# Kernel optimization log

Measured on AMD Instinct MI355X. Metric: run time of the kernel, lower is better.

The kernel has to match this reference:

```python
import jax, jax.numpy as jnp
import numpy as np

# ---- static config (seq_lens / is_prefill are Python lists in the original) ----
HIDDEN, H, D = 4096, 32, 128
SEQ = 1024            # prefill length / decode history length
N_PRE, N_DEC = 4, 4
T = N_PRE * SEQ + N_DEC            # 4100 total tokens
SEQ_LENS = [SEQ] * N_PRE + [SEQ] * N_DEC
IS_PREFILL = [True] * N_PRE + [False] * N_DEC
NUM_SLOTS = 8192
MAX_LEN, ROPE_BASE = 8192, 10000.0
SCALE = D ** -0.5


def _rope_tables():
    inv_freq = 1.0 / (ROPE_BASE ** (np.arange(0, D, 2, dtype=np.float32) / D))
    t = np.arange(MAX_LEN, dtype=np.float32)
    freqs = np.outer(t, inv_freq)
    emb = np.concatenate([freqs, freqs], axis=-1)  # [MAX_LEN, D]
    return jnp.asarray(np.cos(emb), jnp.float32), jnp.asarray(np.sin(emb), jnp.float32)

COS_T, SIN_T = _rope_tables()


def rotate_half(x):
    x1, x2 = jnp.split(x, 2, axis=-1)
    return jnp.concatenate([-x2, x1], axis=-1)


def setup_inputs() -> dict:
    key = jax.random.key(0)
    k1, k2, k3 = jax.random.split(key, 3)
    x = jax.random.normal(k1, (T, HIDDEN), jnp.float32)
    # positions: prefill seqs get 0..SEQ-1, decode seqs are at position SEQ
    pos = np.concatenate([np.tile(np.arange(SEQ), N_PRE), np.full(N_DEC, SEQ)]).astype(np.int64)
    positions = jnp.asarray(pos)
    slot_mapping = jnp.arange(T, dtype=jnp.int64)
    k_cache = jnp.zeros((NUM_SLOTS, H, D), jnp.float32)
    v_cache = jnp.zeros((NUM_SLOTS, H, D), jnp.float32)
    w_qkv = jax.random.normal(k2, (HIDDEN, 3 * H * D), jnp.float32) * 0.02
    w_out = jax.random.normal(k3, (H * D, HIDDEN), jnp.float32) * 0.02
    return {"x": x, "k_cache": k_cache, "v_cache": v_cache, "w_qkv": w_qkv,
            "w_out": w_out, "positions": positions, "slot_mapping": slot_mapping}


def reference(x, k_cache, v_cache, w_qkv, w_out, positions, slot_mapping):
    qkv = x @ w_qkv                                   # [T, 3*H*D]
    q, k, v = jnp.split(qkv, 3, axis=-1)
    q = q.reshape(T, H, D)
    k = k.reshape(T, H, D)
    v = v.reshape(T, H, D)
    cos = COS_T[positions][:, None, :]                # [T, 1, D]
    sin = SIN_T[positions][:, None, :]
    q = q * cos + rotate_half(q) * sin
    k = k * cos + rotate_half(k) * sin
    # scatter new k/v into flat paged cache
    kc = k_cache.at[slot_mapping].set(k)
    vc = v_cache.at[slot_mapping].set(v)

    outs = []
    off = 0
    for seq_len, prefill in zip(SEQ_LENS, IS_PREFILL):
        nq = seq_len if prefill else 1
        q_i = q[off:off + nq]                         # [nq, H, D]
        if prefill:
            k_i, v_i = k[off:off + nq], v[off:off + nq]
            attn = jnp.einsum('qhd,khd->hqk', q_i, k_i) * SCALE
            mask = jnp.triu(jnp.full((nq, nq), -jnp.inf, jnp.float32), 1)
            attn = jax.nn.softmax(attn + mask, axis=-1)
            out = jnp.einsum('hqk,khd->qhd', attn, v_i).reshape(nq, H * D)
        else:
            k_h, v_h = kc[:seq_len], vc[:seq_len]     # history from cache
            attn = jnp.einsum('qhd,khd->hqk', q_i, k_h) * SCALE
            attn = jax.nn.softmax(attn, axis=-1)
            out = jnp.einsum('hqk,khd->qhd', attn, v_h).reshape(1, H * D)
        outs.append(out)
        off += nq
    return jnp.concatenate(outs, axis=0) @ w_out      # [T, HIDDEN]
```

## Files before the change

### kernel.cpp

```cpp
#include <hip/hip_runtime.h>

#define T_TOK 4100
#define MMAIN 4096
#define HID   4096
#define NH    32
#define DH    128
#define NQKV  12288
#define ATT_SCALE 0.08838834764831845f
#define NEG_BIG  (-3.0e38f)

typedef unsigned short ushort_t;
typedef __attribute__((ext_vector_type(8))) short bf16x8;
typedef __attribute__((ext_vector_type(4))) float f32x4;

typedef const void __attribute__((address_space(1)))* gas_ptr;
typedef void __attribute__((address_space(3)))* las_ptr;

__device__ __forceinline__ ushort_t f2bf(float f){
  unsigned int u = __builtin_bit_cast(unsigned int, f);
  u = u + 0x7FFFu + ((u >> 16) & 1u);
  return (ushort_t)(u >> 16);
}
__device__ __forceinline__ float bf2f(ushort_t h){
  unsigned int u = ((unsigned int)h) << 16;
  return __builtin_bit_cast(float, u);
}
__device__ __forceinline__ f32x4 mfma16(bf16x8 a, bf16x8 b, f32x4 c){
  return __builtin_amdgcn_mfma_f32_16x16x32_bf16(a, b, c, 0, 0, 0);
}
__device__ __forceinline__ void gload_lds16(const void* g, void* l){
  __builtin_amdgcn_global_load_lds((gas_ptr)g, (las_ptr)l, 16, 0, 0);
}


__global__ void convert_x(const float* __restrict__ x, ushort_t* __restrict__ xb){
  const long nvec = (long)T_TOK * HID / 4;
  for (long i4 = (long)blockIdx.x * 256 + threadIdx.x; i4 < nvec; i4 += 2048L * 256){
    const long i = i4 * 4;
    const float4 v = *(const float4*)(x + i);
    union { ushort_t u[4]; uint2 w; } o;
    o.u[0] = f2bf(v.x); o.u[1] = f2bf(v.y); o.u[2] = f2bf(v.z); o.u[3] = f2bf(v.w);
    *(uint2*)(xb + i) = o.w;
  }
}

__global__ void tconv(const float* __restrict__ W, ushort_t* __restrict__ WT, int R, int C){
  __shared__ float tile[64][65];
  const int bc = blockIdx.x, br = blockIdx.y;
  const int tid = threadIdx.x;
  const int c4 = tid & 15, r0 = tid >> 4;
  const long cbase = (long)bc * 64 + c4 * 4;
#pragma unroll
  for (int j = 0; j < 4; ++j){
    const int r = r0 + j*16;
    const float4 v = *(const float4*)(W + ((long)br*64 + r) * C + cbase);
    tile[r][c4*4+0] = v.x; tile[r][c4*4+1] = v.y;
    tile[r][c4*4+2] = v.z; tile[r][c4*4+3] = v.w;
  }
  __syncthreads();
  const int c = tid >> 2, rseg = (tid & 3) * 16;
  union { ushort_t u[16]; uint4 w[2]; } o;
#pragma unroll
  for (int e = 0; e < 16; ++e) o.u[e] = f2bf(tile[rseg + e][c]);
  ushort_t* dst = WT + ((long)bc*64 + c) * R + (long)br*64 + rseg;
  *(uint4*)(dst)     = o.w[0];
  *(uint4*)(dst + 8) = o.w[1];
}


#define MFMAQ(QM,QN,BARR)                                                         \
  _Pragma("unroll")                                                               \
  for (int mi = 0; mi < 4; ++mi) {                                                \
    _Pragma("unroll")                                                             \
    for (int ni = 0; ni < 2; ++ni) {                                              \
      acc[QM][QN][mi][ni] = mfma16(af[mi][0], BARR[ni][0], acc[QM][QN][mi][ni]);  \
      acc[QM][QN][mi][ni] = mfma16(af[mi][1], BARR[ni][1], acc[QM][QN][mi][ni]);  \
    } }

template<bool OUT_BF16>
__global__ void __launch_bounds__(512, 2)
gemm256(const ushort_t* __restrict__ A, const ushort_t* __restrict__ B,
        ushort_t* __restrict__ Cb, float* __restrict__ Cf,
        int N, int K, int GM, int Mvalid)
{
  extern __shared__ char smem[];
  char* smA = smem;
  char* smB = smem + 65536;

  const int nwg = gridDim.x;
  int bid = blockIdx.x;
  bid = (bid & 7) * (nwg >> 3) + (bid >> 3);
  const int bm = bid % GM, bn = bid / GM;

  const int tid = threadIdx.x;
  const int wid = tid >> 6, lane = tid & 63;
  const int wm = wid >> 2, wn = wid & 3;
  const int l16 = lane & 15, g = lane >> 4;
  const int lr = lane >> 3, lu = lane & 7;

  const long arow0 = (long)bm * 256;
  const long brow0 = (long)bn * 256;

  const ushort_t* aS[4]; const ushort_t* bS[4];
#pragma unroll
  for (int cc = 0; cc < 4; ++cc){
    aS[cc] = A + (arow0 + cc*64 + wid*8 + lr) * (long)K + (lu ^ lr) * 8;
    bS[cc] = B + (brow0 + cc*64 + wid*8 + lr) * (long)K + (lu ^ lr) * 8;
  }

  auto stageA = [&](int buf, int cc, long kt){
    gload_lds16(aS[cc] + kt, smA + buf*32768 + (cc*64 + wid*8)*128);
  };
  auto stageB = [&](int buf, int cc, long kt){
    gload_lds16(bS[cc] + kt, smB + buf*32768 + (cc*64 + wid*8)*128);
  };
  auto ldA = [&](int buf, int qm, int mi, int ks) -> bf16x8 {
    const int row = qm*128 + wm*64 + mi*16 + l16;
    return *(const bf16x8*)(smA + buf*32768 + row*128 + (((ks*4+g) ^ (l16&7))*16));
  };
  auto ldB = [&](int buf, int qn, int ni, int ks) -> bf16x8 {
    const int row = qn*128 + wn*32 + ni*16 + l16;
    return *(const bf16x8*)(smB + buf*32768 + row*128 + (((ks*4+g) ^ (l16&7))*16));
  };

  f32x4 acc[2][2][4][2];
#pragma unroll
  for (int a_ = 0; a_ < 2; ++a_)
#pragma unroll
  for (int b_ = 0; b_ < 2; ++b_)
#pragma unroll
  for (int c_ = 0; c_ < 4; ++c_)
#pragma unroll
  for (int d_ = 0; d_ < 2; ++d_) acc[a_][b_][c_][d_] = (f32x4){0.f,0.f,0.f,0.f};

  bf16x8 af[4][2], bf0[2][2], bf1[2][2];
  const int NT = K >> 6;

  stageA(0,0,0); stageA(0,1,0);
  stageB(0,0,0); stageB(0,1,0);
  stageB(0,2,0); stageB(0,3,0);
  stageA(0,2,0); stageA(0,3,0);
  asm volatile("s_waitcnt vmcnt(4)" ::: "memory");
  __builtin_amdgcn_s_barrier();

  auto tile = [&](int buf, long ktn){
    asm volatile("s_waitcnt vmcnt(2)" ::: "memory");
#pragma unroll
    for (int mi = 0; mi < 4; ++mi){ af[mi][0] = ldA(buf,0,mi,0); af[mi][1] = ldA(buf,0,mi,1); }
#pragma unroll
    for (int ni = 0; ni < 2; ++ni){ bf0[ni][0] = ldB(buf,0,ni,0); bf0[ni][1] = ldB(buf,0,ni,1); }
    stageA(buf^1, 0, ktn); stageA(buf^1, 1, ktn);
    __builtin_amdgcn_s_barrier();
    asm volatile("s_waitcnt lgkmcnt(0)" ::: "memory");
    __builtin_amdgcn_sched_barrier(0);
    __builtin_amdgcn_s_setprio(1);
    MFMAQ(0,0,bf0);
    __builtin_amdgcn_s_setprio(0);
    asm volatile("s_waitcnt vmcnt(2)" ::: "memory");
#pragma unroll
    for (int ni = 0; ni < 2; ++ni){ bf1[ni][0] = ldB(buf,1,ni,0); bf1[ni][1] = ldB(buf,1,ni,1); }
    stageB(buf^1, 0, ktn); stageB(buf^1, 1, ktn);
    __builtin_amdgcn_s_barrier();
    asm volatile("s_waitcnt lgkmcnt(0)" ::: "memory");
    __builtin_amdgcn_sched_barrier(0);
    __builtin_amdgcn_s_setprio(1);
    MFMAQ(0,1,bf1);
    __builtin_amdgcn_s_setprio(0);
#pragma unroll
    for (int mi = 0; mi < 4; ++mi){ af[mi][0] = ldA(buf,1,mi,0); af[mi][1] = ldA(buf,1,mi,1); }
    stageB(buf^1, 2, ktn); stageB(buf^1, 3, ktn);
    __builtin_amdgcn_s_barrier();
    asm volatile("s_waitcnt lgkmcnt(0)" ::: "memory");
    __builtin_amdgcn_sched_barrier(0);
    __builtin_amdgcn_s_setprio(1);
    MFMAQ(1,1,bf1);
    __builtin_amdgcn_s_setprio(0);
    asm volatile("s_waitcnt vmcnt(2)" ::: "memory");
    stageA(buf^1, 2, ktn); stageA(buf^1, 3, ktn);
    __builtin_amdgcn_s_barrier();
    __builtin_amdgcn_sched_barrier(0);
    __builtin_amdgcn_s_setprio(1);
    MFMAQ(1,0,bf0);
    __builtin_amdgcn_s_setprio(0);
  };

  for (int t = 0; t < NT; t += 2){
    const long k1 = (long)(t+1) * 64;
    const long k2 = (long)((t+2 < NT) ? (t+2) : (NT-1)) * 64;
    tile(0, k1);
    tile(1, k2);
  }
  asm volatile("s_waitcnt vmcnt(0)" ::: "memory");

#pragma unroll
  for (int qm = 0; qm < 2; ++qm)
#pragma unroll
  for (int qn = 0; qn < 2; ++qn)
#pragma unroll
  for (int mi = 0; mi < 4; ++mi)
#pragma unroll
  for (int ni = 0; ni < 2; ++ni)
#pragma unroll
  for (int r = 0; r < 4; ++r){
    const long row = arow0 + qm*128 + wm*64 + mi*16 + g*4 + r;
    const long col = brow0 + qn*128 + wn*32 + ni*16 + l16;
    if (OUT_BF16){
      Cb[row * N + col] = f2bf(acc[qm][qn][mi][ni][r]);
    } else {
      if (row < Mvalid) Cf[row * N + col] = acc[qm][qn][mi][ni][r];
    }
  }
}


__global__ void __launch_bounds__(256, 8)
gemv_tail(const ushort_t* __restrict__ A, const ushort_t* __restrict__ B,
          ushort_t* __restrict__ Cb, float* __restrict__ Cf, int ldc)
{
  const int col  = blockIdx.x * 4 + (threadIdx.x >> 6);
  const int lane = threadIdx.x & 63;
  const ushort_t* brow  = B + (long)col * HID + lane * 64;
  const ushort_t* abase = A + 4096L * HID + lane * 64;
  float acc0 = 0.f, acc1 = 0.f, acc2 = 0.f, acc3 = 0.f;
#pragma unroll
  for (int i = 0; i < 8; ++i){
    union { bf16x8 v; short s[8]; } bv, a0, a1, a2, a3;
    bv.v = *(const bf16x8*)(brow + i*8);
    a0.v = *(const bf16x8*)(abase + 0L*HID + i*8);
    a1.v = *(const bf16x8*)(abase + 1L*HID + i*8);
    a2.v = *(const bf16x8*)(abase + 2L*HID + i*8);
    a3.v = *(const bf16x8*)(abase + 3L*HID + i*8);
#pragma unroll
    for (int e = 0; e < 8; ++e){
      const float bf_ = bf2f((ushort_t)bv.s[e]);
      acc0 += bf2f((ushort_t)a0.s[e]) * bf_;
      acc1 += bf2f((ushort_t)a1.s[e]) * bf_;
      acc2 += bf2f((ushort_t)a2.s[e]) * bf_;
      acc3 += bf2f((ushort_t)a3.s[e]) * bf_;
    }
  }
#pragma unroll
  for (int off = 32; off; off >>= 1){
    acc0 += __shfl_xor(acc0, off);
    acc1 += __shfl_xor(acc1, off);
    acc2 += __shfl_xor(acc2, off);
    acc3 += __shfl_xor(acc3, off);
  }
  if (lane == 0){
    if (Cb){
      Cb[4096L*ldc + col] = f2bf(acc0);
      Cb[4097L*ldc + col] = f2bf(acc1);
      Cb[4098L*ldc + col] = f2bf(acc2);
      Cb[4099L*ldc + col] = f2bf(acc3);
    } else {
      Cf[4096L*ldc + col] = acc0;
      Cf[4097L*ldc + col] = acc1;
      Cf[4098L*ldc + col] = acc2;
      Cf[4099L*ldc + col] = acc3;
    }
  }
}


__global__ void rope_scatter(ushort_t* __restrict__ qkv,
                             const int* __restrict__ pos32,
                             const int* __restrict__ slot32,
                             ushort_t* __restrict__ kcw, ushort_t* __restrict__ vcw)
{
  const long gi = (long)blockIdx.x * 256 + threadIdx.x;
  if (gi >= (long)T_TOK * NH * 8) return;
  const int  i8 = gi & 7;
  const int  h  = (gi >> 3) & 31;
  const long t  = gi >> 8;

  const bool p64 = (pos32[1] == 0);
  const bool s64 = (slot32[1] == 0);
  const long pv   = p64 ? ((const long long*)pos32)[t]  : (long)pos32[t];
  const long slot = s64 ? ((const long long*)slot32)[t] : (long)slot32[t];

  float cs[8], sn[8];
#pragma unroll
  for (int e = 0; e < 8; ++e){
    const int i = i8*8 + e;
    const float inv = exp2f(-(float)i * 0.2076187116f);
    __sincosf((float)pv * inv, &sn[e], &cs[e]);
  }

  ushort_t* base = qkv + t * (long)NQKV + h * DH + i8*8;
  {
    union { bf16x8 v; short s[8]; } lo, hi;
    lo.v = *(const bf16x8*)(base);
    hi.v = *(const bf16x8*)(base + 64);
#pragma unroll
    for (int e = 0; e < 8; ++e){
      const float a = bf2f((ushort_t)lo.s[e]), b = bf2f((ushort_t)hi.s[e]);
      lo.s[e] = (short)f2bf(a * cs[e] - b * sn[e]);
      hi.s[e] = (short)f2bf(b * cs[e] + a * sn[e]);
    }
    *(bf16x8*)(base)      = lo.v;
    *(bf16x8*)(base + 64) = hi.v;
  }

  if (t < 4096){
    ushort_t* kb = base + HID;
    union { bf16x8 v; short s[8]; } lo, hi;
    lo.v = *(const bf16x8*)(kb);
    hi.v = *(const bf16x8*)(kb + 64);
#pragma unroll
    for (int e = 0; e < 8; ++e){
      const float a = bf2f((ushort_t)lo.s[e]), b = bf2f((ushort_t)hi.s[e]);
      lo.s[e] = (short)f2bf(a * cs[e] - b * sn[e]);
      hi.s[e] = (short)f2bf(b * cs[e] + a * sn[e]);
    }
    *(bf16x8*)(kb)      = lo.v;
    *(bf16x8*)(kb + 64) = hi.v;

    if (slot >= 0 && slot < 1024){
      ushort_t* kd = kcw + (slot * NH + h) * DH + i8*8;
      *(bf16x8*)(kd)      = lo.v;
      *(bf16x8*)(kd + 64) = hi.v;
      const ushort_t* vsrc = base + 2 * HID;
      ushort_t* vd = vcw + (slot * NH + h) * DH + i8*8;
      *(bf16x8*)(vd)      = *(const bf16x8*)(vsrc);
      *(bf16x8*)(vd + 64) = *(const bf16x8*)(vsrc + 64);
    }
  }
}


__global__ void __launch_bounds__(256, 3)
attn_fused(const ushort_t* __restrict__ qkv, const ushort_t* __restrict__ kcw,
           const ushort_t* __restrict__ vcw, ushort_t* __restrict__ attn)
{
  __shared__ char sm[44032];
  const int qb = blockIdx.x, h = blockIdx.y, sq = blockIdx.z;
  const int tid = threadIdx.x, wid = tid >> 6, lane = tid & 63;

  if (qb == 16){
    float* qs  = (float*)sm;
    float* ps  = qs + 128;
    float* red = ps + 1024;
    float* oh  = red + 8;
    const long t = 4096 + sq;
    if (tid < 128) qs[tid] = bf2f(qkv[t * (long)NQKV + h*DH + tid]);
    __syncthreads();
    float sv[4];
#pragma unroll
    for (int j = 0; j < 4; j++){
      const int key = tid + j*256;
      const ushort_t* kr = kcw + ((long)key * NH + h) * DH;
      float acc = 0.f;
      for (int d = 0; d < 128; d += 8){
        union { bf16x8 v; short s8[8]; } uu;
        uu.v = *(const bf16x8*)(kr + d);
#pragma unroll
        for (int e = 0; e < 8; e++) acc += qs[d+e] * bf2f((ushort_t)uu.s8[e]);
      }
      sv[j] = acc * ATT_SCALE;
    }
    float mx = fmaxf(fmaxf(sv[0], sv[1]), fmaxf(sv[2], sv[3]));
#pragma unroll
    for (int off = 1; off < 64; off <<= 1) mx = fmaxf(mx, __shfl_xor(mx, off));
    if (lane == 0) red[wid] = mx;
    __syncthreads();
    const float gmax = fmaxf(fmaxf(red[0], red[1]), fmaxf(red[2], red[3]));
    float psum = 0.f;
#pragma unroll
    for (int j = 0; j < 4; j++){
      const float p = __expf(sv[j] - gmax);
      ps[tid + j*256] = p;
      psum += p;
    }
#pragma unroll
    for (int off = 1; off < 64; off <<= 1) psum += __shfl_xor(psum, off);
    if (lane == 0) red[4 + wid] = psum;
    __syncthreads();
    const float gsum = red[4] + red[5] + red[6] + red[7];
    const int d = tid & 127, half = tid >> 7;
    float acc = 0.f;
    for (int key = half*512; key < half*512 + 512; ++key)
      acc += ps[key] * bf2f(vcw[((long)key * NH + h) * DH + d]);
    if (half) oh[d] = acc;
    __syncthreads();
    if (!half) attn[t * HID + h*DH + d] = f2bf((acc + oh[d]) / gsum);
    return;
  }

  ushort_t (*Ks)[128]    = (ushort_t(*)[128])sm;
  ushort_t (*Vt)[72]     = (ushort_t(*)[72])(sm + 16384);
  ushort_t (*Ps)[16][72] = (ushort_t(*)[16][72])(sm + 34816);
  const long tok0 = (long)sq * 1024;
  const int l16 = lane & 15, g = lane >> 4;
  const int q0 = qb * 64;

  bf16x8 qf[4];
  {
    const ushort_t* qrow = qkv + (tok0 + q0 + wid*16 + l16) * (long)NQKV + h * DH;
#pragma unroll
    for (int dc = 0; dc < 4; ++dc) qf[dc] = *(const bf16x8*)(qrow + dc*32 + g*8);
  }

  bf16x8 vones;
  {
    union { ushort_t u[8]; bf16x8 v; } one_;
#pragma unroll
    for (int e = 0; e < 8; ++e) one_.u[e] = 0x3F80;
    vones = one_.v;
  }

  f32x4 oacc[8];
#pragma unroll
  for (int i = 0; i < 8; i++) oacc[i] = (f32x4){0.f, 0.f, 0.f, 0.f};
  f32x4 lacc = (f32x4){0.f, 0.f, 0.f, 0.f};

  const int nkb = qb + 1;
  for (int kb = 0; kb < nkb; ++kb){
    __syncthreads();
    {
      const ushort_t* kbase = qkv + (tok0 + kb*64) * (long)NQKV + HID + h * DH;
#pragma unroll
      for (int c = 0; c < 4; ++c){
        const int row = c*16 + wid*4 + g;
        const int pu = (l16 & 8) | ((l16 ^ (row & 7)) & 7);
        gload_lds16(kbase + (long)row * NQKV + pu*8, &Ks[c*16 + wid*4][0]);
      }
    }
    {
      const int key4 = (tid & 15) * 4;
      const int dg8  = tid >> 4;
      const ushort_t* vbase = qkv + (tok0 + kb*64) * (long)NQKV + 2*HID + h*DH + dg8*8;
      union { bf16x8 v; short s8[8]; } vr[4];
#pragma unroll
      for (int j = 0; j < 4; ++j)
        vr[j].v = *(const bf16x8*)(vbase + (long)(key4 + j) * NQKV);
#pragma unroll
      for (int e = 0; e < 8; ++e){
        union { ushort_t u[4]; uint2 w; } o;
        o.u[0] = (ushort_t)vr[0].s8[e]; o.u[1] = (ushort_t)vr[1].s8[e];
        o.u[2] = (ushort_t)vr[2].s8[e]; o.u[3] = (ushort_t)vr[3].s8[e];
        *(uint2*)&Vt[dg8*8 + e][key4] = o.w;
      }
    }
    __syncthreads();

    {
      f32x4 sfr[4];
#pragma unroll
      for (int nf = 0; nf < 4; ++nf) sfr[nf] = (f32x4){0.f,0.f,0.f,0.f};
      __builtin_amdgcn_s_setprio(1);
#pragma unroll
      for (int nf = 0; nf < 4; ++nf){
#pragma unroll
        for (int dc = 0; dc < 4; ++dc){
          const int uu = dc*4 + g;
          const int pu = (uu & 8) | ((uu ^ (l16 & 7)) & 7);
          bf16x8 kf = *(const bf16x8*)&Ks[nf*16 + l16][pu * 8];
          sfr[nf] = mfma16(qf[dc], kf, sfr[nf]);
        }
      }
      __builtin_amdgcn_s_setprio(0);
      const bool diag = (kb == qb);
#pragma unroll
      for (int r = 0; r < 4; r++){
        float s4[4];
#pragma unroll
        for (int nf = 0; nf < 4; ++nf) s4[nf] = sfr[nf][r] * ATT_SCALE;
        if (diag){
          const int qg = q0 + wid*16 + g*4 + r;
#pragma unroll
          for (int nf = 0; nf < 4; ++nf)
            if (kb*64 + nf*16 + l16 > qg) s4[nf] = NEG_BIG;
        }
#pragma unroll
        for (int nf = 0; nf < 4; ++nf)
          Ps[wid][g*4 + r][nf*16 + l16] = f2bf(__expf(s4[nf]));
      }
      __builtin_amdgcn_s_setprio(1);
#pragma unroll
      for (int ks = 0; ks < 2; ++ks){
        bf16x8 pa = *(const bf16x8*)&Ps[wid][l16][ks*32 + g*8];
        lacc = mfma16(pa, vones, lacc);
#pragma unroll
        for (int df = 0; df < 8; ++df){
          bf16x8 vf = *(const bf16x8*)&Vt[df*16 + l16][ks*32 + g*8];
          oacc[df] = mfma16(pa, vf, oacc[df]);
        }
      }
      __builtin_amdgcn_s_setprio(0);
    }
  }

#pragma unroll
  for (int df = 0; df < 8; ++df){
#pragma unroll
    for (int r = 0; r < 4; ++r){
      const long row = tok0 + q0 + wid*16 + g*4 + r;
      attn[row * HID + h*DH + df*16 + l16] = f2bf(oacc[df][r] / lacc[r]);
    }
  }
}


extern "C" void kernel_launch(void* const* d_in, const int* in_sizes, int n_in,
                              void* d_out, int out_size, void* d_ws, size_t ws_size,
                              hipStream_t stream) {
  const float* x      = (const float*)d_in[0];
  const float* wqkv   = (const float*)d_in[3];
  const float* wout   = (const float*)d_in[4];
  const int*   pos    = (const int*)d_in[5];
  const int*   slots  = (const int*)d_in[6];

  char* ws = (char*)d_ws;
  ushort_t* xb    = (ushort_t*)(ws);
  ushort_t* qkvb  = (ushort_t*)(ws + 35651584L);
  ushort_t* wqkvT = (ushort_t*)(ws + 142606336L);
  ushort_t* attnb = (ushort_t*)(ws + 142606336L);
  ushort_t* woutT = (ushort_t*)(ws + 243269632L);
  ushort_t* kcw   = (ushort_t*)(ws + 276824064L);
  ushort_t* vcw   = (ushort_t*)(ws + 285212672L);

  hipFuncSetAttribute((const void*)gemm256<true>,
                      hipFuncAttributeMaxDynamicSharedMemorySize, 131072);
  hipFuncSetAttribute((const void*)gemm256<false>,
                      hipFuncAttributeMaxDynamicSharedMemorySize, 131072);

  convert_x<<<2048, 256, 0, stream>>>(x, xb);
  tconv<<<dim3(NQKV/64, HID/64), 256, 0, stream>>>(wqkv, wqkvT, HID, NQKV);
  tconv<<<dim3(HID/64, HID/64), 256, 0, stream>>>(wout, woutT, HID, HID);

  gemm256<true><<<(MMAIN/256)*(NQKV/256), 512, 131072, stream>>>(
      xb, wqkvT, qkvb, nullptr, NQKV, HID, MMAIN/256, MMAIN);
  gemv_tail<<<HID/4, 256, 0, stream>>>(xb, wqkvT, qkvb, nullptr, NQKV);

  rope_scatter<<<4100, 256, 0, stream>>>(qkvb, pos, slots, kcw, vcw);

  attn_fused<<<dim3(17, NH, 4), 256, 0, stream>>>(qkvb, kcw, vcw, attnb);

  gemm256<false><<<(MMAIN/256)*(HID/256), 512, 131072, stream>>>(
      attnb, woutT, nullptr, (float*)d_out, HID, HID, MMAIN/256, MMAIN);
  gemv_tail<<<HID/4, 256, 0, stream>>>(attnb, woutT, nullptr, (float*)d_out, HID);

  (void)in_sizes; (void)n_in; (void)out_size; (void)ws_size;
}
```

Before: 812.5 us.

## Merge prep kernels, add GEMM phase barriers, reverse attention block order

Folds the x-to-bf16 conversion and both weight transpose-converts into one launch, cutting launch overhead and letting the three prep jobs overlap. Adds an s_barrier after each MFMA quadrant in the GEMM main loop so the waves stay in lockstep, which may cut LDS contention but adds sync stalls. Reverses the causal attention query-block order so the heaviest blocks are dispatched first, for better load balance.

```diff
diff --git a/kernel.cpp b/kernel.cpp
--- a/kernel.cpp
+++ b/kernel.cpp
@@ -33,21 +33,10 @@
 }
 
 
-__global__ void convert_x(const float* __restrict__ x, ushort_t* __restrict__ xb){
-  const long nvec = (long)T_TOK * HID / 4;
-  for (long i4 = (long)blockIdx.x * 256 + threadIdx.x; i4 < nvec; i4 += 2048L * 256){
-    const long i = i4 * 4;
-    const float4 v = *(const float4*)(x + i);
-    union { ushort_t u[4]; uint2 w; } o;
-    o.u[0] = f2bf(v.x); o.u[1] = f2bf(v.y); o.u[2] = f2bf(v.z); o.u[3] = f2bf(v.w);
-    *(uint2*)(xb + i) = o.w;
-  }
-}
-
-__global__ void tconv(const float* __restrict__ W, ushort_t* __restrict__ WT, int R, int C){
+__device__ __forceinline__ void tconv_body(const float* __restrict__ W,
+                                           ushort_t* __restrict__ WT,
+                                           int R, int C, int bc, int br, int tid){
   __shared__ float tile[64][65];
-  const int bc = blockIdx.x, br = blockIdx.y;
-  const int tid = threadIdx.x;
   const int c4 = tid & 15, r0 = tid >> 4;
   const long cbase = (long)bc * 64 + c4 * 4;
 #pragma unroll
@@ -65,6 +54,27 @@
   ushort_t* dst = WT + ((long)bc*64 + c) * R + (long)br*64 + rseg;
   *(uint4*)(dst)     = o.w[0];
   *(uint4*)(dst + 8) = o.w[1];
+}
+
+__global__ void prep(const float* __restrict__ x, ushort_t* __restrict__ xb,
+                     const float* __restrict__ wqkv, ushort_t* __restrict__ wqkvT,
+                     const float* __restrict__ wout, ushort_t* __restrict__ woutT){
+  const int b = blockIdx.x, tid = threadIdx.x;
+  if (b < 12288){
+    tconv_body(wqkv, wqkvT, HID, NQKV, b % 192, b / 192, tid);
+  } else if (b < 16384){
+    const int t = b - 12288;
+    tconv_body(wout, woutT, HID, HID, t % 64, t / 64, tid);
+  } else {
+    const long nvec = (long)T_TOK * HID / 4;
+    for (long i4 = (long)(b - 16384) * 256 + tid; i4 < nvec; i4 += 512L * 256){
+      const long i = i4 * 4;
+      const float4 v = *(const float4*)(x + i);
+      union { ushort_t u[4]; uint2 w; } o;
+      o.u[0] = f2bf(v.x); o.u[1] = f2bf(v.y); o.u[2] = f2bf(v.z); o.u[3] = f2bf(v.w);
+      *(uint2*)(xb + i) = o.w;
+    }
+  }
 }
 
 
@@ -156,6 +166,7 @@
     __builtin_amdgcn_s_setprio(1);
     MFMAQ(0,0,bf0);
     __builtin_amdgcn_s_setprio(0);
+    __builtin_amdgcn_s_barrier();
     asm volatile("s_waitcnt vmcnt(2)" ::: "memory");
 #pragma unroll
     for (int ni = 0; ni < 2; ++ni){ bf1[ni][0] = ldB(buf,1,ni,0); bf1[ni][1] = ldB(buf,1,ni,1); }
@@ -166,6 +177,7 @@
     __builtin_amdgcn_s_setprio(1);
     MFMAQ(0,1,bf1);
     __builtin_amdgcn_s_setprio(0);
+    __builtin_amdgcn_s_barrier();
 #pragma unroll
     for (int mi = 0; mi < 4; ++mi){ af[mi][0] = ldA(buf,1,mi,0); af[mi][1] = ldA(buf,1,mi,1); }
     stageB(buf^1, 2, ktn); stageB(buf^1, 3, ktn);
@@ -175,6 +187,7 @@
     __builtin_amdgcn_s_setprio(1);
     MFMAQ(1,1,bf1);
     __builtin_amdgcn_s_setprio(0);
+    __builtin_amdgcn_s_barrier();
     asm volatile("s_waitcnt vmcnt(2)" ::: "memory");
     stageA(buf^1, 2, ktn); stageA(buf^1, 3, ktn);
     __builtin_amdgcn_s_barrier();
@@ -182,6 +195,7 @@
     __builtin_amdgcn_s_setprio(1);
     MFMAQ(1,0,bf0);
     __builtin_amdgcn_s_setprio(0);
+    __builtin_amdgcn_s_barrier();
   };
 
   for (int t = 0; t < NT; t += 2){
@@ -333,10 +347,10 @@
            const ushort_t* __restrict__ vcw, ushort_t* __restrict__ attn)
 {
   __shared__ char sm[44032];
-  const int qb = blockIdx.x, h = blockIdx.y, sq = blockIdx.z;
+  const int bx = blockIdx.x, h = blockIdx.y, sq = blockIdx.z;
   const int tid = threadIdx.x, wid = tid >> 6, lane = tid & 63;
 
-  if (qb == 16){
+  if (bx == 16){
     float* qs  = (float*)sm;
     float* ps  = qs + 128;
     float* red = ps + 1024;
@@ -389,6 +403,7 @@
   ushort_t (*Ks)[128]    = (ushort_t(*)[128])sm;
   ushort_t (*Vt)[72]     = (ushort_t(*)[72])(sm + 16384);
   ushort_t (*Ps)[16][72] = (ushort_t(*)[16][72])(sm + 34816);
+  const int qb = 15 - bx;
   const long tok0 = (long)sq * 1024;
   const int l16 = lane & 15, g = lane >> 4;
   const int q0 = qb * 64;
@@ -524,9 +539,7 @@
   hipFuncSetAttribute((const void*)gemm256<false>,
                       hipFuncAttributeMaxDynamicSharedMemorySize, 131072);
 
-  convert_x<<<2048, 256, 0, stream>>>(x, xb);
-  tconv<<<dim3(NQKV/64, HID/64), 256, 0, stream>>>(wqkv, wqkvT, HID, NQKV);
-  tconv<<<dim3(HID/64, HID/64), 256, 0, stream>>>(wout, woutT, HID, HID);
+  prep<<<16896, 256, 0, stream>>>(x, xb, wqkv, wqkvT, wout, woutT);
 
   gemm256<true><<<(MMAIN/256)*(NQKV/256), 512, 131072, stream>>>(
       xb, wqkvT, qkvb, nullptr, NQKV, HID, MMAIN/256, MMAIN);
```

New measurement: 847.3 us. 4.3% more time.
